# Performance work log

Hardware: AMD Instinct MI355X
Metric: run time of the kernel (lower is better)

## Reference

```python
import jax, jax.numpy as jnp
import numpy as np

CUTOFF = 2.0
LOG2 = float(np.log(2.0))

def ssp(x):
    # shifted softplus: softplus(x) - log(2)
    return jax.nn.softplus(x) - LOG2

def setup_inputs() -> dict:
    key = jax.random.key(0)
    ks = jax.random.split(key, 12)
    N, E, H, F, G = 10000, 320000, 256, 256, 50
    x = jax.random.normal(ks[0], (N, H), dtype=jnp.float32)
    edge_index = jax.random.randint(ks[1], (2, E), 0, N, dtype=jnp.int64)
    edge_weight = jax.random.normal(ks[2], (E, 3), dtype=jnp.float32)
    edge_attr = jax.random.normal(ks[3], (E, G), dtype=jnp.float32)
    s = lambda fan_in: 1.0 / np.sqrt(fan_in)
    mlp_w1 = jax.random.uniform(ks[4], (G, F), jnp.float32, -s(G), s(G))
    mlp_b1 = jax.random.uniform(ks[5], (F,), jnp.float32, -s(G), s(G))
    mlp_w2 = jax.random.uniform(ks[6], (F, F), jnp.float32, -s(F), s(F))
    mlp_b2 = jax.random.uniform(ks[7], (F,), jnp.float32, -s(F), s(F))
    lin1_w = jax.random.uniform(ks[8], (H, F), jnp.float32, -s(H), s(H))
    lin2_w = jax.random.uniform(ks[9], (F, H), jnp.float32, -s(F), s(F))
    lin2_b = jax.random.uniform(ks[10], (H,), jnp.float32, -s(F), s(F))
    return {"x": x, "edge_index": edge_index, "edge_weight": edge_weight,
            "edge_attr": edge_attr, "mlp_w1": mlp_w1, "mlp_b1": mlp_b1,
            "mlp_w2": mlp_w2, "mlp_b2": mlp_b2, "lin1_w": lin1_w,
            "lin2_w": lin2_w, "lin2_b": lin2_b}

def reference(x, edge_index, edge_weight, edge_attr,
              mlp_w1, mlp_b1, mlp_w2, mlp_b2, lin1_w, lin2_w, lin2_b):
    N = x.shape[0]
    # cutoff envelope on edge distances
    distances = jnp.linalg.norm(edge_weight, axis=1)                 # [E]
    C = 0.5 * (jnp.cos(distances * jnp.pi / CUTOFF) + 1.0)
    C = C * (distances <= CUTOFF)                                    # [E]
    # edge filter MLP
    W = ssp(edge_attr @ mlp_w1 + mlp_b1) @ mlp_w2 + mlp_b2           # [E, F]
    W = W * C[:, None]
    i, j = edge_index[0], edge_index[1]
    messages = W * (x[j] @ lin1_w)                                   # [E, F]
    agg = jax.ops.segment_sum(messages, i, num_segments=N)           # [N, F]
    h = ssp(agg @ lin2_w + lin2_b)                                   # [N, H]
    return x + h
```

## Files before the change

### kernel.cpp

```cpp
#include <hip/hip_runtime.h>
#include <hip/hip_bf16.h>
#include <stdint.h>

#define HF 256
#define GG 50

typedef __attribute__((ext_vector_type(8))) short bf16x8;
typedef __attribute__((ext_vector_type(4))) short bf16x4;
typedef __attribute__((ext_vector_type(4))) float f32x4;

__device__ __forceinline__ uint32_t f2bf2u(float a, float b){
    __hip_bfloat162 h = __float22bfloat162_rn(make_float2(a, b));
    union { __hip_bfloat162 h; uint32_t u; } v; v.h = h; return v.u;
}
__device__ __forceinline__ float bf2f(short s){
    union { uint32_t u; float f; } v; v.u = ((uint32_t)(uint16_t)s) << 16;
    return v.f;
}
__device__ __forceinline__ float ssp_f(float x){
    return fmaxf(x, 0.f) + __logf(1.f + __expf(-fabsf(x))) - 0.69314718055994531f;
}

__device__ __forceinline__ void pack_natural(const float* __restrict__ B,
                                             short* __restrict__ Bp,
                                             int idx, int KT, int kmax)
{
    int lane = idx & 63;
    int kt   = (idx >> 6) & (KT - 1);
    int ntg  = idx >> (6 + (KT == 2 ? 1 : 3));
    int col  = ntg * 16 + (lane & 15);
    int k0   = kt * 32 + (lane >> 4) * 8;
    uint32_t u[4];
#pragma unroll
    for (int jj = 0; jj < 4; ++jj) {
        int ka = k0 + 2*jj, kb = ka + 1;
        float a = (ka < kmax) ? B[(size_t)ka * HF + col] : 0.f;
        float b = (kb < kmax) ? B[(size_t)kb * HF + col] : 0.f;
        u[jj] = f2bf2u(a, b);
    }
    *(uint4*)&Bp[(size_t)idx * 8] = *(uint4*)u;
}

__global__ __launch_bounds__(256)
void prep_kernel(const float* __restrict__ w1, const float* __restrict__ w2,
                 const float* __restrict__ lin1, const float* __restrict__ lin2,
                 short* __restrict__ w1p, short* __restrict__ w2p,
                 short* __restrict__ lin1p, short* __restrict__ lin2p,
                 const float* __restrict__ x, short* __restrict__ x_bf, int nx8,
                 const int* __restrict__ eidx, int* __restrict__ cnt, int E,
                 float* __restrict__ agg, int nAgg4, int gConv, int gHist)
{
    int b = blockIdx.x, tid = threadIdx.x;
    if (b < 8) {
        pack_natural(w1, w1p, b * 256 + tid, 2, GG);
    } else if (b < 40) {
        int idx = (b - 8) * 256 + tid;
        int lane = idx & 63;
        int kt   = (idx >> 6) & 7;
        int ntg  = idx >> 9;
        int col  = ntg * 16 + (lane & 15);
        int s0   = kt * 32 + (lane >> 4) * 8;
        uint32_t u[4];
#pragma unroll
        for (int jj = 0; jj < 4; ++jj) {
            int sa = s0 + 2*jj, sb = sa + 1;
            int fa = (sa >> 6) * 64 + (sa & 3) * 16 + ((sa & 63) >> 2);
            int fb = (sb >> 6) * 64 + (sb & 3) * 16 + ((sb & 63) >> 2);
            u[jj] = f2bf2u(w2[(size_t)fa * HF + col], w2[(size_t)fb * HF + col]);
        }
        *(uint4*)&w2p[(size_t)idx * 8] = *(uint4*)u;
    } else if (b < 72) {
        pack_natural(lin1, lin1p, (b - 40) * 256 + tid, 8, HF);
    } else if (b < 104) {
        pack_natural(lin2, lin2p, (b - 72) * 256 + tid, 8, HF);
    } else if (b < 104 + gConv) {
        int idx = (b - 104) * 256 + tid;
        if (idx < nx8) {
            const float* xp = x + (size_t)idx * 8;
            float4 p0 = *(const float4*)(xp);
            float4 p1 = *(const float4*)(xp + 4);
            uint32_t u[4] = { f2bf2u(p0.x, p0.y), f2bf2u(p0.z, p0.w),
                              f2bf2u(p1.x, p1.y), f2bf2u(p1.z, p1.w) };
            *(uint4*)&x_bf[(size_t)idx * 8] = *(uint4*)u;
        }
    } else if (b < 104 + gConv + gHist) {
        int e = (b - 104 - gConv) * 256 + tid;
        if (e < E) atomicAdd(&cnt[eidx[e]], 1);
    } else {
        int idx = (b - 104 - gConv - gHist) * 256 + tid;
        if (idx < nAgg4) ((float4*)agg)[idx] = make_float4(0.f, 0.f, 0.f, 0.f);
    }
}

__global__ __launch_bounds__(256)
void scan_kernel(const int* __restrict__ cnt, int* __restrict__ row,
                 int* __restrict__ cursor, int N, int E)
{
    __shared__ int part[256];
    const int t = threadIdx.x;
    const int CH = (N + 255) / 256;
    int lo = t * CH;
    int hi = min(lo + CH, N);
    int s = 0;
    for (int n = lo; n < hi; ++n) s += cnt[n];
    part[t] = s;
    __syncthreads();
    for (int off = 1; off < 256; off <<= 1) {
        int v = (t >= off) ? part[t - off] : 0;
        __syncthreads();
        part[t] += v;
        __syncthreads();
    }
    int acc = part[t] - s;
    for (int n = lo; n < hi; ++n) {
        row[n] = acc; cursor[n] = acc;
        acc += cnt[n];
    }
    if (t == 255) row[N] = E;
}

__global__ __launch_bounds__(256)
void mid_kernel(const int* __restrict__ eidx, int* __restrict__ cursor,
                int* __restrict__ perm, int E, int gScatter,
                const short* __restrict__ x_bf, const short* __restrict__ lin1p,
                short* __restrict__ y_p, int N)
{
    const int tid = threadIdx.x;
    if ((int)blockIdx.x < gScatter) {
        int e = blockIdx.x * 256 + tid;
        if (e < E) {
            int pos = atomicAdd(&cursor[eidx[e]], 1);
            perm[pos] = e;
        }
        return;
    }
    const int blk  = blockIdx.x - gScatter;
    const int lane = tid & 63;
    const int w    = tid >> 6;
    const int l15  = lane & 15;
    const int quad = lane >> 4;
    const int row0 = blk * 64;

    f32x4 acc[4][4];
#pragma unroll
    for (int mt = 0; mt < 4; ++mt)
#pragma unroll
        for (int nt = 0; nt < 4; ++nt) acc[mt][nt] = (f32x4){0.f,0.f,0.f,0.f};

#pragma unroll 2
    for (int kt = 0; kt < 8; ++kt) {
        bf16x8 af[4];
#pragma unroll
        for (int mt = 0; mt < 4; ++mt) {
            int r = row0 + mt * 16 + l15;
            int rl = (r < N) ? r : 0;
            af[mt] = *(const bf16x8*)&x_bf[(size_t)rl * HF + kt * 32 + quad * 8];
        }
#pragma unroll
        for (int nt = 0; nt < 4; ++nt) {
            bf16x8 bfr = *(const bf16x8*)&lin1p[(size_t)(((w*4+nt)*8+kt)*64+lane)*8];
#pragma unroll
            for (int mt = 0; mt < 4; ++mt)
                acc[mt][nt] = __builtin_amdgcn_mfma_f32_16x16x32_bf16(af[mt], bfr, acc[mt][nt], 0, 0, 0);
        }
    }
#pragma unroll
    for (int mt = 0; mt < 4; ++mt) {
#pragma unroll
        for (int r = 0; r < 4; ++r) {
            int row = row0 + mt * 16 + quad * 4 + r;
            if (row < N) {
                uint2 u = make_uint2(f2bf2u(acc[mt][0][r], acc[mt][1][r]),
                                     f2bf2u(acc[mt][2][r], acc[mt][3][r]));
                *(uint2*)&y_p[(size_t)row * HF + w * 64 + l15 * 4] = u;
            }
        }
    }
}

__global__ __launch_bounds__(256)
void node2_kernel(const float* __restrict__ agg, const short* __restrict__ lin2p,
                  const float* __restrict__ bias, const float* __restrict__ x,
                  float* __restrict__ out, int N)
{
    const int tid  = threadIdx.x;
    const int lane = tid & 63;
    const int w    = tid >> 6;
    const int l15  = lane & 15;
    const int quad = lane >> 4;
    const int row0 = blockIdx.x * 64;

    f32x4 acc[4][4];
#pragma unroll
    for (int mt = 0; mt < 4; ++mt)
#pragma unroll
        for (int nt = 0; nt < 4; ++nt) acc[mt][nt] = (f32x4){0.f,0.f,0.f,0.f};

#pragma unroll 2
    for (int kt = 0; kt < 8; ++kt) {
        bf16x8 af[4];
#pragma unroll
        for (int mt = 0; mt < 4; ++mt) {
            int r = row0 + mt * 16 + l15;
            int rl = (r < N) ? r : 0;
            const float* ap = agg + (size_t)rl * HF + kt * 32 + quad * 8;
            float4 p0 = *(const float4*)(ap);
            float4 p1 = *(const float4*)(ap + 4);
            union { uint32_t u[4]; bf16x8 v; } c;
            c.u[0] = f2bf2u(p0.x, p0.y); c.u[1] = f2bf2u(p0.z, p0.w);
            c.u[2] = f2bf2u(p1.x, p1.y); c.u[3] = f2bf2u(p1.z, p1.w);
            af[mt] = c.v;
        }
#pragma unroll
        for (int nt = 0; nt < 4; ++nt) {
            bf16x8 bfr = *(const bf16x8*)&lin2p[(size_t)(((w*4+nt)*8+kt)*64+lane)*8];
#pragma unroll
            for (int mt = 0; mt < 4; ++mt)
                acc[mt][nt] = __builtin_amdgcn_mfma_f32_16x16x32_bf16(af[mt], bfr, acc[mt][nt], 0, 0, 0);
        }
    }
    float bs[4];
#pragma unroll
    for (int nt = 0; nt < 4; ++nt) bs[nt] = bias[w * 64 + nt * 16 + l15];
#pragma unroll
    for (int mt = 0; mt < 4; ++mt) {
#pragma unroll
        for (int r = 0; r < 4; ++r) {
            int row = row0 + mt * 16 + quad * 4 + r;
            if (row < N) {
#pragma unroll
                for (int nt = 0; nt < 4; ++nt) {
                    int f = w * 64 + nt * 16 + l15;
                    float v = ssp_f(acc[mt][nt][r] + bs[nt]) + x[(size_t)row * HF + f];
                    out[(size_t)row * HF + f] = v;
                }
            }
        }
    }
}

__global__ __launch_bounds__(256, 3)
void edge_mfma(const float* __restrict__ ea, const int* __restrict__ eidx,
               const float* __restrict__ ew,
               const short* __restrict__ w1p, const float* __restrict__ b1,
               const short* __restrict__ w2p, const float* __restrict__ b2,
               const short* __restrict__ y_p, const int* __restrict__ perm,
               const int* __restrict__ rowp,
               float* __restrict__ agg, int E)
{
    __shared__ short smem[21504];
    short* ea_b = smem;
    short* hid  = smem + 4608;
    short* msgT = smem;
    short* St   = smem + 18432;
    __shared__ int s_e[64], s_i[64], s_j[64];
    __shared__ float s_c[64];
    __shared__ int s_runnode[64];
    __shared__ unsigned char s_runcomp[64];
    __shared__ unsigned long long s_bmask;
    __shared__ int s_runcnt;

    const int tid  = threadIdx.x;
    const int lane = tid & 63;
    const int w    = tid >> 6;
    const int l15  = lane & 15;
    const int quad = lane >> 4;
    const int e0   = blockIdx.x * 64;

    if (tid < 64) {
        int pp = e0 + tid;
        int e = 0, iv = -1, jv = 0;
        float c = 0.f;
        if (pp < E) {
            e  = perm[pp];
            iv = eidx[e];
            jv = eidx[E + e];
            float d0 = ew[e*3+0], d1 = ew[e*3+1], d2 = ew[e*3+2];
            float d = sqrtf(d0*d0 + d1*d1 + d2*d2);
            c = (d <= 2.0f) ? 0.5f * (__cosf(d * 1.57079632679489662f) + 1.0f) : 0.f;
        }
        s_e[tid] = e; s_i[tid] = iv; s_j[tid] = jv; s_c[tid] = c;
        int ivn = __shfl_down(iv, 1);
        bool flag = (tid == 63) || (iv != ivn);
        unsigned long long m = __ballot(flag);
        if (flag) {
            int rid = (int)__popcll(m & ((1ull << tid) - 1ull));
            s_runnode[rid] = iv;
            int comp = 0;
            if (iv >= 0) {
                int lo = rowp[iv], hi = rowp[iv + 1];
                comp = (lo >= e0 && hi <= e0 + 64) ? 1 : 0;
            }
            s_runcomp[rid] = (unsigned char)comp;
        }
        if (tid == 0) { s_bmask = m; s_runcnt = (int)__popcll(m); }
    }
    __syncthreads();

    for (int idx = tid; idx < 64 * 25; idx += 256) {
        int e = idx / 25, q = idx - e * 25;
        const float* sp = ea + (size_t)s_e[e] * GG + q * 2;
        float2 v = *(const float2*)sp;
        *(uint32_t*)&ea_b[e * 72 + q * 2] = f2bf2u(v.x, v.y);
    }
    for (int idx = tid; idx < 64 * 7; idx += 256) {
        int e = idx / 7, q = idx - e * 7;
        *(uint32_t*)&ea_b[e * 72 + 50 + q * 2] = 0u;
    }
    __syncthreads();

    f32x4 acc1[4][4];
#pragma unroll
    for (int mt = 0; mt < 4; ++mt)
#pragma unroll
        for (int nt = 0; nt < 4; ++nt) acc1[mt][nt] = (f32x4){0.f,0.f,0.f,0.f};

#pragma unroll
    for (int kt = 0; kt < 2; ++kt) {
        bf16x8 af[4];
#pragma unroll
        for (int mt = 0; mt < 4; ++mt)
            af[mt] = *(bf16x8*)&ea_b[(mt * 16 + l15) * 72 + kt * 32 + quad * 8];
#pragma unroll
        for (int nt = 0; nt < 4; ++nt) {
            bf16x8 bfr = *(const bf16x8*)&w1p[(size_t)(((w*4+nt)*2+kt)*64+lane)*8];
#pragma unroll
            for (int mt = 0; mt < 4; ++mt)
                acc1[mt][nt] = __builtin_amdgcn_mfma_f32_16x16x32_bf16(af[mt], bfr, acc1[mt][nt], 0, 0, 0);
        }
    }

    float bias1[4];
#pragma unroll
    for (int nt = 0; nt < 4; ++nt) bias1[nt] = b1[w * 64 + nt * 16 + l15];
#pragma unroll
    for (int mt = 0; mt < 4; ++mt) {
#pragma unroll
        for (int r = 0; r < 4; ++r) {
            int e = mt * 16 + quad * 4 + r;
            float v0 = ssp_f(acc1[mt][0][r] + bias1[0]);
            float v1 = ssp_f(acc1[mt][1][r] + bias1[1]);
            float v2 = ssp_f(acc1[mt][2][r] + bias1[2]);
            float v3 = ssp_f(acc1[mt][3][r] + bias1[3]);
            uint2 u = make_uint2(f2bf2u(v0, v1), f2bf2u(v2, v3));
            *(uint2*)&hid[e * 264 + w * 64 + l15 * 4] = u;
        }
    }
    __syncthreads();

    bf16x4 yv[4][4];
#pragma unroll
    for (int mt = 0; mt < 4; ++mt)
#pragma unroll
        for (int r = 0; r < 4; ++r) {
            int e = mt * 16 + quad * 4 + r;
            yv[mt][r] = *(const bf16x4*)&y_p[(size_t)s_j[e] * HF + w * 64 + l15 * 4];
        }

    f32x4 acc2[4][4];
#pragma unroll
    for (int mt = 0; mt < 4; ++mt)
#pragma unroll
        for (int nt = 0; nt < 4; ++nt) acc2[mt][nt] = (f32x4){0.f,0.f,0.f,0.f};

#pragma unroll 2
    for (int kt = 0; kt < 8; ++kt) {
        bf16x8 af[4];
#pragma unroll
        for (int mt = 0; mt < 4; ++mt)
            af[mt] = *(bf16x8*)&hid[(mt * 16 + l15) * 264 + kt * 32 + quad * 8];
#pragma unroll
        for (int nt = 0; nt < 4; ++nt) {
            bf16x8 bfr = *(const bf16x8*)&w2p[(size_t)(((w*4+nt)*8+kt)*64+lane)*8];
#pragma unroll
            for (int mt = 0; mt < 4; ++mt)
                acc2[mt][nt] = __builtin_amdgcn_mfma_f32_16x16x32_bf16(af[mt], bfr, acc2[mt][nt], 0, 0, 0);
        }
    }
    __syncthreads();

    float bias2[4];
#pragma unroll
    for (int nt = 0; nt < 4; ++nt) bias2[nt] = b2[w * 64 + nt * 16 + l15];
    float cs[4][4];
#pragma unroll
    for (int mt = 0; mt < 4; ++mt)
#pragma unroll
        for (int r = 0; r < 4; ++r)
            cs[mt][r] = s_c[mt * 16 + quad * 4 + r];
#pragma unroll
    for (int mt = 0; mt < 4; ++mt) {
#pragma unroll
        for (int nt = 0; nt < 4; ++nt) {
            int col = w * 64 + nt * 16 + l15;
            float v0 = (acc2[mt][nt][0] + bias2[nt]) * cs[mt][0] * bf2f(yv[mt][0][nt]);
            float v1 = (acc2[mt][nt][1] + bias2[nt]) * cs[mt][1] * bf2f(yv[mt][1][nt]);
            float v2 = (acc2[mt][nt][2] + bias2[nt]) * cs[mt][2] * bf2f(yv[mt][2][nt]);
            float v3 = (acc2[mt][nt][3] + bias2[nt]) * cs[mt][3] * bf2f(yv[mt][3][nt]);
            uint2 u = make_uint2(f2bf2u(v0, v1), f2bf2u(v2, v3));
            *(uint2*)&msgT[col * 72 + mt * 16 + quad * 4] = u;
        }
    }
    {
        unsigned long long bm = s_bmask;
        int e   = tid & 63;
        int rb  = tid >> 6;
        int rid = (int)__popcll(bm & ((1ull << e) - 1ull));
#pragma unroll
        for (int q = 0; q < 4; ++q) {
            int r = rb + q * 4;
            St[r * 64 + e] = (rid == r) ? (short)0x3F80 : (short)0;
        }
    }
    __syncthreads();

    const int runcnt = s_runcnt;
    for (int ntg = 0; ntg * 16 < runcnt; ++ntg) {
        if (ntg > 0) {
            __syncthreads();
            unsigned long long bm = s_bmask;
            int e   = tid & 63;
            int rb  = tid >> 6;
            int rid = (int)__popcll(bm & ((1ull << e) - 1ull));
#pragma unroll
            for (int q = 0; q < 4; ++q) {
                int r = rb + q * 4;
                St[r * 64 + e] = (rid == ntg * 16 + r) ? (short)0x3F80 : (short)0;
            }
            __syncthreads();
        }
        f32x4 acc3[4];
#pragma unroll
        for (int mt = 0; mt < 4; ++mt) acc3[mt] = (f32x4){0.f,0.f,0.f,0.f};
#pragma unroll
        for (int kt = 0; kt < 2; ++kt) {
            bf16x8 bS = *(bf16x8*)&St[l15 * 64 + kt * 32 + quad * 8];
#pragma unroll
            for (int mt = 0; mt < 4; ++mt) {
                bf16x8 af = *(bf16x8*)&msgT[(w*64 + mt*16 + l15) * 72 + kt*32 + quad*8];
                acc3[mt] = __builtin_amdgcn_mfma_f32_16x16x32_bf16(af, bS, acc3[mt], 0, 0, 0);
            }
        }
        int r = ntg * 16 + l15;
        if (r < runcnt) {
            int node = s_runnode[r];
            if (node >= 0) {
                float* ap = agg + (size_t)node * HF + w * 64 + quad * 4;
                if (s_runcomp[r]) {
#pragma unroll
                    for (int mt = 0; mt < 4; ++mt) {
                        float4 v = make_float4(acc3[mt][0], acc3[mt][1], acc3[mt][2], acc3[mt][3]);
                        *(float4*)(ap + mt * 16) = v;
                    }
                } else {
#pragma unroll
                    for (int mt = 0; mt < 4; ++mt)
#pragma unroll
                        for (int g = 0; g < 4; ++g)
                            atomicAdd(ap + mt * 16 + g, acc3[mt][g]);
                }
            }
        }
    }
}

extern "C" void kernel_launch(void* const* d_in, const int* in_sizes, int n_in,
                              void* d_out, int out_size, void* d_ws, size_t ws_size,
                              hipStream_t stream)
{
    const float* x     = (const float*)d_in[0];
    const int*   eidx  = (const int*)  d_in[1];
    const float* ew    = (const float*)d_in[2];
    const float* ea    = (const float*)d_in[3];
    const float* w1    = (const float*)d_in[4];
    const float* b1    = (const float*)d_in[5];
    const float* w2    = (const float*)d_in[6];
    const float* b2    = (const float*)d_in[7];
    const float* lin1  = (const float*)d_in[8];
    const float* lin2  = (const float*)d_in[9];
    const float* lin2b = (const float*)d_in[10];
    float* out = (float*)d_out;

    const int N = in_sizes[0] / HF;
    const int E = in_sizes[2] / 3;

    const size_t fN = (size_t)N * HF;
    float* agg    = (float*)d_ws;
    short* y_p    = (short*)(agg + fN);
    short* x_bf   = y_p + fN;
    int*   cnt    = (int*)(x_bf + fN);
    int*   row    = cnt + N;
    int*   cursor = row + (N + 8);
    int*   perm   = cursor + N;
    short* w1p    = (short*)(((uintptr_t)(perm + E) + 255) & ~(uintptr_t)255);
    short* w2p    = w1p + 16384;
    short* lin1p  = w2p + 65536;
    short* lin2p  = lin1p + 65536;

    hipMemsetAsync(cnt, 0, (size_t)N * sizeof(int), stream);

    const int nx8   = (int)(fN / 8);
    const int nAgg4 = (int)(fN / 4);
    const int gConv = (nx8 + 255) / 256;
    const int gHist = (E + 255) / 256;
    const int gZero = (nAgg4 + 255) / 256;
    prep_kernel<<<dim3(104 + gConv + gHist + gZero), dim3(256), 0, stream>>>(
        w1, w2, lin1, lin2, w1p, w2p, lin1p, lin2p, x, x_bf, nx8,
        eidx, cnt, E, agg, nAgg4, gConv, gHist);

    scan_kernel<<<dim3(1), dim3(256), 0, stream>>>(cnt, row, cursor, N, E);

    const int gScatter = (E + 255) / 256;
    const int gNode    = (N + 63) / 64;
    mid_kernel<<<dim3(gScatter + gNode), dim3(256), 0, stream>>>(
        eidx, cursor, perm, E, gScatter, x_bf, lin1p, y_p, N);

    edge_mfma<<<dim3((E + 63) / 64), dim3(256), 0, stream>>>(
        ea, eidx, ew, w1p, b1, w2p, b2, y_p, perm, row, agg, E);

    node2_kernel<<<dim3(gNode), dim3(256), 0, stream>>>(
        agg, lin2p, lin2b, x, out, N);
}
```

Baseline: 351.6 us.

## Fold MLP bias into GEMM, alias LDS buffers, shrink node tiles, cheaper softplus

The first-layer bias is folded into the edge-filter GEMM by packing b1 as an extra K row and writing a constant 1.0 column into the padded edge-attribute tile. The hidden buffer now aliases the ea_b buffer, with an added barrier, so LDS use drops and occupancy can rise to 4 blocks per SIMD. The two node GEMM kernels use 32-row tiles to launch more blocks. ssp is rewritten with exp2/log hardware intrinsics, dropping the |x| stabilization, which risks overflow of exp for large inputs and some loss of accuracy.

```diff
diff --git a/kernel.cpp b/kernel.cpp
--- a/kernel.cpp
+++ b/kernel.cpp
@@ -18,7 +18,9 @@
     return v.f;
 }
 __device__ __forceinline__ float ssp_f(float x){
-    return fmaxf(x, 0.f) + __logf(1.f + __expf(-fabsf(x))) - 0.69314718055994531f;
+    float e = __builtin_amdgcn_exp2f(x * 1.44269504088896341f);
+    return 0.69314718055994531f * __builtin_amdgcn_logf(1.0f + e)
+         - 0.69314718055994531f;
 }
 
 __device__ __forceinline__ void pack_natural(const float* __restrict__ B,
@@ -42,7 +44,8 @@
 }
 
 __global__ __launch_bounds__(256)
-void prep_kernel(const float* __restrict__ w1, const float* __restrict__ w2,
+void prep_kernel(const float* __restrict__ w1, const float* __restrict__ b1,
+                 const float* __restrict__ w2,
                  const float* __restrict__ lin1, const float* __restrict__ lin2,
                  short* __restrict__ w1p, short* __restrict__ w2p,
                  short* __restrict__ lin1p, short* __restrict__ lin2p,
@@ -52,7 +55,23 @@
 {
     int b = blockIdx.x, tid = threadIdx.x;
     if (b < 8) {
-        pack_natural(w1, w1p, b * 256 + tid, 2, GG);
+        int idx  = b * 256 + tid;
+        int lane = idx & 63;
+        int kt   = (idx >> 6) & 1;
+        int ntg  = idx >> 7;
+        int col  = ntg * 16 + (lane & 15);
+        int k0   = kt * 32 + (lane >> 4) * 8;
+        uint32_t u[4];
+#pragma unroll
+        for (int jj = 0; jj < 4; ++jj) {
+            int ka = k0 + 2*jj, kb = ka + 1;
+            float va = (ka < GG) ? w1[(size_t)ka * HF + col]
+                                 : ((ka == GG) ? b1[col] : 0.f);
+            float vb = (kb < GG) ? w1[(size_t)kb * HF + col]
+                                 : ((kb == GG) ? b1[col] : 0.f);
+            u[jj] = f2bf2u(va, vb);
+        }
+        *(uint4*)&w1p[(size_t)idx * 8] = *(uint4*)u;
     } else if (b < 40) {
         int idx = (b - 8) * 256 + tid;
         int lane = idx & 63;
@@ -139,19 +158,19 @@
     const int w    = tid >> 6;
     const int l15  = lane & 15;
     const int quad = lane >> 4;
-    const int row0 = blk * 64;
-
-    f32x4 acc[4][4];
-#pragma unroll
-    for (int mt = 0; mt < 4; ++mt)
+    const int row0 = blk * 32;
+
+    f32x4 acc[2][4];
+#pragma unroll
+    for (int mt = 0; mt < 2; ++mt)
 #pragma unroll
         for (int nt = 0; nt < 4; ++nt) acc[mt][nt] = (f32x4){0.f,0.f,0.f,0.f};
 
 #pragma unroll 2
     for (int kt = 0; kt < 8; ++kt) {
-        bf16x8 af[4];
-#pragma unroll
-        for (int mt = 0; mt < 4; ++mt) {
+        bf16x8 af[2];
+#pragma unroll
+        for (int mt = 0; mt < 2; ++mt) {
             int r = row0 + mt * 16 + l15;
             int rl = (r < N) ? r : 0;
             af[mt] = *(const bf16x8*)&x_bf[(size_t)rl * HF + kt * 32 + quad * 8];
@@ -160,12 +179,12 @@
         for (int nt = 0; nt < 4; ++nt) {
             bf16x8 bfr = *(const bf16x8*)&lin1p[(size_t)(((w*4+nt)*8+kt)*64+lane)*8];
 #pragma unroll
-            for (int mt = 0; mt < 4; ++mt)
+            for (int mt = 0; mt < 2; ++mt)
                 acc[mt][nt] = __builtin_amdgcn_mfma_f32_16x16x32_bf16(af[mt], bfr, acc[mt][nt], 0, 0, 0);
         }
     }
 #pragma unroll
-    for (int mt = 0; mt < 4; ++mt) {
+    for (int mt = 0; mt < 2; ++mt) {
 #pragma unroll
         for (int r = 0; r < 4; ++r) {
             int row = row0 + mt * 16 + quad * 4 + r;
@@ -188,19 +207,19 @@
     const int w    = tid >> 6;
     const int l15  = lane & 15;
     const int quad = lane >> 4;
-    const int row0 = blockIdx.x * 64;
-
-    f32x4 acc[4][4];
-#pragma unroll
-    for (int mt = 0; mt < 4; ++mt)
+    const int row0 = blockIdx.x * 32;
+
+    f32x4 acc[2][4];
+#pragma unroll
+    for (int mt = 0; mt < 2; ++mt)
 #pragma unroll
         for (int nt = 0; nt < 4; ++nt) acc[mt][nt] = (f32x4){0.f,0.f,0.f,0.f};
 
 #pragma unroll 2
     for (int kt = 0; kt < 8; ++kt) {
-        bf16x8 af[4];
-#pragma unroll
-        for (int mt = 0; mt < 4; ++mt) {
+        bf16x8 af[2];
+#pragma unroll
+        for (int mt = 0; mt < 2; ++mt) {
             int r = row0 + mt * 16 + l15;
             int rl = (r < N) ? r : 0;
             const float* ap = agg + (size_t)rl * HF + kt * 32 + quad * 8;
@@ -215,7 +234,7 @@
         for (int nt = 0; nt < 4; ++nt) {
             bf16x8 bfr = *(const bf16x8*)&lin2p[(size_t)(((w*4+nt)*8+kt)*64+lane)*8];
 #pragma unroll
-            for (int mt = 0; mt < 4; ++mt)
+            for (int mt = 0; mt < 2; ++mt)
                 acc[mt][nt] = __builtin_amdgcn_mfma_f32_16x16x32_bf16(af[mt], bfr, acc[mt][nt], 0, 0, 0);
         }
     }
@@ -223,7 +242,7 @@
 #pragma unroll
     for (int nt = 0; nt < 4; ++nt) bs[nt] = bias[w * 64 + nt * 16 + l15];
 #pragma unroll
-    for (int mt = 0; mt < 4; ++mt) {
+    for (int mt = 0; mt < 2; ++mt) {
 #pragma unroll
         for (int r = 0; r < 4; ++r) {
             int row = row0 + mt * 16 + quad * 4 + r;
@@ -239,18 +258,18 @@
     }
 }
 
-__global__ __launch_bounds__(256, 3)
+__global__ __launch_bounds__(256, 4)
 void edge_mfma(const float* __restrict__ ea, const int* __restrict__ eidx,
                const float* __restrict__ ew,
-               const short* __restrict__ w1p, const float* __restrict__ b1,
+               const short* __restrict__ w1p,
                const short* __restrict__ w2p, const float* __restrict__ b2,
                const short* __restrict__ y_p, const int* __restrict__ perm,
                const int* __restrict__ rowp,
                float* __restrict__ agg, int E)
 {
-    __shared__ short smem[21504];
+    __shared__ short smem[19456];
     short* ea_b = smem;
-    short* hid  = smem + 4608;
+    short* hid  = smem;
     short* msgT = smem;
     short* St   = smem + 18432;
     __shared__ int s_e[64], s_i[64], s_j[64];
@@ -305,7 +324,7 @@
     }
     for (int idx = tid; idx < 64 * 7; idx += 256) {
         int e = idx / 7, q = idx - e * 7;
-        *(uint32_t*)&ea_b[e * 72 + 50 + q * 2] = 0u;
+        *(uint32_t*)&ea_b[e * 72 + 50 + q * 2] = (q == 0) ? 0x00003F80u : 0u;
     }
     __syncthreads();
 
@@ -329,19 +348,17 @@
                 acc1[mt][nt] = __builtin_amdgcn_mfma_f32_16x16x32_bf16(af[mt], bfr, acc1[mt][nt], 0, 0, 0);
         }
     }
-
-    float bias1[4];
-#pragma unroll
-    for (int nt = 0; nt < 4; ++nt) bias1[nt] = b1[w * 64 + nt * 16 + l15];
+    __syncthreads();
+
 #pragma unroll
     for (int mt = 0; mt < 4; ++mt) {
 #pragma unroll
         for (int r = 0; r < 4; ++r) {
             int e = mt * 16 + quad * 4 + r;
-            float v0 = ssp_f(acc1[mt][0][r] + bias1[0]);
-            float v1 = ssp_f(acc1[mt][1][r] + bias1[1]);
-            float v2 = ssp_f(acc1[mt][2][r] + bias1[2]);
-            float v3 = ssp_f(acc1[mt][3][r] + bias1[3]);
+            float v0 = ssp_f(acc1[mt][0][r]);
+            float v1 = ssp_f(acc1[mt][1][r]);
+            float v2 = ssp_f(acc1[mt][2][r]);
+            float v3 = ssp_f(acc1[mt][3][r]);
             uint2 u = make_uint2(f2bf2u(v0, v1), f2bf2u(v2, v3));
             *(uint2*)&hid[e * 264 + w * 64 + l15 * 4] = u;
         }
@@ -505,18 +522,18 @@
     const int gHist = (E + 255) / 256;
     const int gZero = (nAgg4 + 255) / 256;
     prep_kernel<<<dim3(104 + gConv + gHist + gZero), dim3(256), 0, stream>>>(
-        w1, w2, lin1, lin2, w1p, w2p, lin1p, lin2p, x, x_bf, nx8,
+        w1, b1, w2, lin1, lin2, w1p, w2p, lin1p, lin2p, x, x_bf, nx8,
         eidx, cnt, E, agg, nAgg4, gConv, gHist);
 
     scan_kernel<<<dim3(1), dim3(256), 0, stream>>>(cnt, row, cursor, N, E);
 
     const int gScatter = (E + 255) / 256;
-    const int gNode    = (N + 63) / 64;
+    const int gNode    = (N + 31) / 32;
     mid_kernel<<<dim3(gScatter + gNode), dim3(256), 0, stream>>>(
         eidx, cursor, perm, E, gScatter, x_bf, lin1p, y_p, N);
 
     edge_mfma<<<dim3((E + 63) / 64), dim3(256), 0, stream>>>(
-        ea, eidx, ew, w1p, b1, w2p, b2, y_p, perm, row, agg, E);
+        ea, eidx, ew, w1p, w2p, b2, y_p, perm, row, agg, E);
 
     node2_kernel<<<dim3(gNode), dim3(256), 0, stream>>>(
         agg, lin2p, lin2b, x, out, N);
```

Measured after the change: 358.9 us. 1.02x slower.
